# Kernel tuning notes

Hardware: AMD Instinct MI355X
Metric: run time of the kernel (lower is better)

Reference implementation:

```python
import jax, jax.numpy as jnp
import numpy as np

NUM_GROUPS = 32
EPS = 1e-6


def setup_inputs() -> dict:
    key = jax.random.key(0)
    ks = jax.random.split(key, 11)
    b, c, h, w = 4, 512, 64, 64
    s = 0.02
    return {
        "x": jax.random.normal(ks[0], (b, c, h, w), dtype=jnp.float32),
        "gn_w": jnp.ones((c,), dtype=jnp.float32),
        "gn_b": jnp.zeros((c,), dtype=jnp.float32),
        "wq": jax.random.normal(ks[1], (c, c), dtype=jnp.float32) * s,
        "bq": jax.random.normal(ks[2], (c,), dtype=jnp.float32) * s,
        "wk": jax.random.normal(ks[3], (c, c), dtype=jnp.float32) * s,
        "bk": jax.random.normal(ks[4], (c,), dtype=jnp.float32) * s,
        "wv": jax.random.normal(ks[5], (c, c), dtype=jnp.float32) * s,
        "bv": jax.random.normal(ks[6], (c,), dtype=jnp.float32) * s,
        "wo": jax.random.normal(ks[7], (c, c), dtype=jnp.float32) * s,
        "bo": jax.random.normal(ks[8], (c,), dtype=jnp.float32) * s,
    }


def _group_norm(x, gamma, beta):
    b, c, h, w = x.shape
    g = NUM_GROUPS
    xg = x.reshape(b, g, c // g, h, w)
    mean = jnp.mean(xg, axis=(2, 3, 4), keepdims=True)
    var = jnp.var(xg, axis=(2, 3, 4), keepdims=True)
    xg = (xg - mean) * jax.lax.rsqrt(var + EPS)
    x = xg.reshape(b, c, h, w)
    return x * gamma[None, :, None, None] + beta[None, :, None, None]


def _conv1x1(x, wmat, bias):
    # x: [b,c,h,w], wmat: [out,in] -> [b,out,h,w]
    return jnp.einsum('bchw,oc->bohw', x, wmat) + bias[None, :, None, None]


def reference(x, gn_w, gn_b, wq, bq, wk, bk, wv, bv, wo, bo):
    b, c, h, w = x.shape
    h_ = _group_norm(x, gn_w, gn_b)
    q = _conv1x1(h_, wq, bq).reshape(b, c, h * w)  # [b,c,hw]
    k = _conv1x1(h_, wk, bk).reshape(b, c, h * w)
    v = _conv1x1(h_, wv, bv).reshape(b, c, h * w)
    scale = float(c) ** (-0.5)
    # scores[b,i,j] = sum_c q[b,c,i] * k[b,c,j]
    scores = jnp.einsum('bci,bcj->bij', q, k) * scale
    attn = jax.nn.softmax(scores, axis=2)  # softmax over j (keys)
    # out[b,c,i] = sum_j v[b,c,j] * attn[b,i,j]
    out = jnp.einsum('bcj,bij->bci', v, attn).reshape(b, c, h, w)
    out = _conv1x1(out, wo, bo)
    return x + out
```

## Files before the change

kernel.cpp:

```cpp
#include <hip/hip_runtime.h>
#include <math.h>

using short8 = __attribute__((ext_vector_type(8))) short;
using f32x4  = __attribute__((ext_vector_type(4))) float;
using llong2 = __attribute__((ext_vector_type(2))) long long;
using i32x8  = __attribute__((ext_vector_type(8))) int;

__device__ __forceinline__ ushort f2bf(float f) {
    union { float f; uint u; } c; c.f = f;
    uint u = c.u;
    uint r = (u + 0x7FFFu + ((u >> 16) & 1u)) >> 16;
    return (ushort)r;
}
__device__ __forceinline__ float bf2f(ushort h) {
    union { uint u; float f; } c; c.u = ((uint)h) << 16;
    return c.f;
}
__device__ __forceinline__ uint pk4_fp8(float a, float b, float c, float d) {
    int v = __builtin_amdgcn_cvt_pk_fp8_f32(a, b, 0, false);
    v = __builtin_amdgcn_cvt_pk_fp8_f32(c, d, v, true);
    return (uint)v;
}
__device__ __forceinline__ unsigned char f2fp8(float x) {
    return (unsigned char)__builtin_amdgcn_cvt_pk_fp8_f32(x, 0.f, 0, false);
}

__device__ __forceinline__ void gload16(const void* g, void* l) {
    __builtin_amdgcn_global_load_lds(
        (const __attribute__((address_space(1))) unsigned int*)g,
        (__attribute__((address_space(3))) unsigned int*)l,
        16, 0, 0);
}

__global__ __launch_bounds__(256) void prep_weights(
    const float* __restrict__ wq, const float* __restrict__ bq,
    const float* __restrict__ wk, const float* __restrict__ bk,
    const float* __restrict__ wv, const float* __restrict__ wo,
    ushort* __restrict__ Wqk, ushort* __restrict__ Wv, ushort* __restrict__ Wo,
    float* __restrict__ bqk, float* __restrict__ stats, float scale)
{
    int idx = blockIdx.x * 256 + threadIdx.x;
    if (idx < 1024 * 512) {
        float v = (idx < 262144) ? wq[idx] * scale : wk[idx - 262144];
        Wqk[idx] = f2bf(v);
    }
    if (idx < 262144) {
        Wv[idx] = f2bf(wv[idx]);
        Wo[idx] = f2bf(wo[idx]);
    }
    if (idx < 1024) bqk[idx] = (idx < 512) ? bq[idx] * scale : bk[idx - 512];
    if (idx < 256) stats[idx] = 0.f;
}

__global__ __launch_bounds__(256) void gn_stats(
    const float* __restrict__ x, float* __restrict__ stats)
{
    int blk = blockIdx.x;
    int grp = blk >> 3, sub = blk & 7;
    const float* xp = x + (size_t)grp * 65536 + sub * 8192;
    int tid = threadIdx.x;

    float s = 0.f, sq = 0.f;
    #pragma unroll
    for (int j = 0; j < 8; ++j) {
        float4 v = *(const float4*)&xp[tid * 4 + j * 1024];
        s  += v.x + v.y + v.z + v.w;
        sq += v.x * v.x + v.y * v.y + v.z * v.z + v.w * v.w;
    }
    #pragma unroll
    for (int off = 32; off; off >>= 1) {
        s  += __shfl_xor(s,  off, 64);
        sq += __shfl_xor(sq, off, 64);
    }
    __shared__ float red[8];
    if ((tid & 63) == 0) { red[(tid >> 6) * 2] = s; red[(tid >> 6) * 2 + 1] = sq; }
    __syncthreads();
    if (tid == 0) {
        atomicAdd(&stats[grp * 2],     red[0] + red[2] + red[4] + red[6]);
        atomicAdd(&stats[grp * 2 + 1], red[1] + red[3] + red[5] + red[7]);
    }
}

__global__ __launch_bounds__(256) void gn_apply(
    const float* __restrict__ x, const float* __restrict__ gamma,
    const float* __restrict__ beta, const float* __restrict__ stats,
    ushort* __restrict__ hnt)
{
    int blk = blockIdx.x;
    int grp = blk >> 4, tile = blk & 15;
    int b = grp >> 5, g = grp & 31;
    const float* xp = x + (size_t)grp * 65536;
    int tid = threadIdx.x;

    float mean = stats[grp * 2] * (1.f / 65536.f);
    float var  = stats[grp * 2 + 1] * (1.f / 65536.f) - mean * mean;
    float rstd = rsqrtf(var + 1e-6f);

    int i0 = tile * 256;
    __shared__ ushort ls[16][256];
    #pragma unroll
    for (int ch = 0; ch < 16; ++ch) {
        float a = rstd * gamma[g * 16 + ch];
        float c = beta[g * 16 + ch] - mean * a;
        ls[ch][tid] = f2bf(xp[ch * 4096 + i0 + tid] * a + c);
    }
    __syncthreads();
    ushort t[16];
    #pragma unroll
    for (int ch = 0; ch < 16; ++ch) t[ch] = ls[ch][tid];
    size_t dst = ((size_t)b * 4096 + i0 + tid) * 512 + g * 16;
    *(uint4*)&hnt[dst]     = *(const uint4*)&t[0];
    *(uint4*)&hnt[dst + 8] = *(const uint4*)&t[8];
}

__global__ __launch_bounds__(256) void softmax_kernel(
    const ushort* __restrict__ S, unsigned char* __restrict__ P8)
{
    size_t row = blockIdx.x;
    const ushort* p = S + row * 4096;
    int tid = threadIdx.x;

    ushort tmp[16];
    *(uint4*)&tmp[0] = *(const uint4*)&p[tid * 16];
    *(uint4*)&tmp[8] = *(const uint4*)&p[tid * 16 + 8];
    float v[16];
    float mx = -1e30f;
    #pragma unroll
    for (int j = 0; j < 16; ++j) { v[j] = bf2f(tmp[j]); mx = fmaxf(mx, v[j]); }
    #pragma unroll
    for (int off = 32; off; off >>= 1) mx = fmaxf(mx, __shfl_xor(mx, off, 64));
    __shared__ float ls[8];
    if ((tid & 63) == 0) ls[tid >> 6] = mx;
    __syncthreads();
    float m4 = fmaxf(fmaxf(ls[0], ls[1]), fmaxf(ls[2], ls[3]));
    float sum = 0.f;
    #pragma unroll
    for (int j = 0; j < 16; ++j) { v[j] = __expf(v[j] - m4); sum += v[j]; }
    #pragma unroll
    for (int off = 32; off; off >>= 1) sum += __shfl_xor(sum, off, 64);
    if ((tid & 63) == 0) ls[4 + (tid >> 6)] = sum;
    __syncthreads();
    float inv = 256.0f / (ls[4] + ls[5] + ls[6] + ls[7]);
    int u = tid & 3;
    size_t base = row * 4096 + (size_t)(tid >> 2) * 64
                + (u & 1) * 32 + (u >> 1) * 8;
    uint2 o0, o1;
    o0.x = pk4_fp8(v[0] * inv,  v[1] * inv,  v[2] * inv,  v[3] * inv);
    o0.y = pk4_fp8(v[4] * inv,  v[5] * inv,  v[6] * inv,  v[7] * inv);
    o1.x = pk4_fp8(v[8] * inv,  v[9] * inv,  v[10] * inv, v[11] * inv);
    o1.y = pk4_fp8(v[12] * inv, v[13] * inv, v[14] * inv, v[15] * inv);
    *(uint2*)&P8[base]      = o0;
    *(uint2*)&P8[base + 16] = o1;
}

template <int BIAS, int OUT>
__global__ __launch_bounds__(256, 4) void gemm_nt(
    const ushort* __restrict__ Ag, const ushort* __restrict__ Bg,
    void* __restrict__ Cv, void* __restrict__ Cv2,
    const float* __restrict__ bias, const float* __restrict__ resid,
    int N, int K, int lda, int ldb,
    long sA, long sB, long sC)
{
    const int bz = blockIdx.z;
    Ag += (size_t)bz * sA;
    Bg += (size_t)bz * sB;

    const int tid  = threadIdx.x;
    const int wave = tid >> 6, lane = tid & 63;
    const int q = lane >> 4, lr = lane & 15;
    const int m0 = blockIdx.x * 128, n0 = blockIdx.y * 128;
    const int wm = (wave >> 1) * 64, wn = (wave & 1) * 64;

    __shared__ __align__(16) ushort As[2][128 * 32];
    __shared__ __align__(16) ushort Bs[2][128 * 32];

    const int srow = wave * 32 + (lane >> 2);
    const int skc  = (lane & 3) << 3;
    const size_t aoff0 = (size_t)(m0 + srow) * lda + skc;
    const size_t aoff1 = aoff0 + (size_t)16 * lda;
    const size_t boff0 = (size_t)(n0 + srow) * ldb + skc;
    const size_t boff1 = boff0 + (size_t)16 * ldb;
    const int l0 = wave * 1024, l1 = wave * 1024 + 512;

    f32x4 acc[4][4] = {};

    for (int kb = 0; kb < K; kb += 64) {
        __syncthreads();
        gload16(&Ag[aoff0 + kb],      &As[0][l0]);
        gload16(&Ag[aoff1 + kb],      &As[0][l1]);
        gload16(&Ag[aoff0 + kb + 32], &As[1][l0]);
        gload16(&Ag[aoff1 + kb + 32], &As[1][l1]);
        gload16(&Bg[boff0 + kb],      &Bs[0][l0]);
        gload16(&Bg[boff1 + kb],      &Bs[0][l1]);
        gload16(&Bg[boff0 + kb + 32], &Bs[1][l0]);
        gload16(&Bg[boff1 + kb + 32], &Bs[1][l1]);
        __syncthreads();

        #pragma unroll
        for (int kh = 0; kh < 2; ++kh) {
            short8 af[4], bfr[4];
            #pragma unroll
            for (int mt = 0; mt < 4; ++mt)
                af[mt] = *(const short8*)&As[kh][(wm + mt * 16 + lr) * 32 + q * 8];
            #pragma unroll
            for (int nt = 0; nt < 4; ++nt)
                bfr[nt] = *(const short8*)&Bs[kh][(wn + nt * 16 + lr) * 32 + q * 8];
            #pragma unroll
            for (int mt = 0; mt < 4; ++mt)
                #pragma unroll
                for (int nt = 0; nt < 4; ++nt)
                    acc[mt][nt] = __builtin_amdgcn_mfma_f32_16x16x32_bf16(
                        af[mt], bfr[nt], acc[mt][nt], 0, 0, 0);
        }
    }

    #pragma unroll
    for (int mt = 0; mt < 4; ++mt) {
        int rb = m0 + wm + mt * 16 + q * 4;
        #pragma unroll
        for (int nt = 0; nt < 4; ++nt) {
            int cn = n0 + wn + nt * 16 + lr;
            #pragma unroll
            for (int t = 0; t < 4; ++t) {
                int r = rb + t;
                float v = acc[mt][nt][t];
                if (BIAS == 1) v += bias[r];
                if (BIAS == 2) v += bias[cn];
                if (OUT == 1) {
                    size_t o = (size_t)bz * sC + (size_t)r * N + cn;
                    ((float*)Cv)[o] = v + resid[o];
                } else if (OUT == 2) {
                    int w = cn & 63, a = w >> 3;
                    int sp = (cn & ~63) | ((a & 3) * 16 + (a >> 2) * 8 + (w & 7));
                    ((unsigned char*)Cv)[(size_t)bz * sC + (size_t)r * N + sp] =
                        f2fp8(v);
                } else if (OUT == 3) {
                    if (cn < 512)
                        ((unsigned char*)Cv)[(size_t)bz * sC + (size_t)r * 512 + cn]
                            = f2fp8(v * 16.f);
                    else
                        ((unsigned char*)Cv2)[(size_t)bz * sC + (size_t)r * 512 + (cn - 512)]
                            = f2fp8(v);
                } else {
                    size_t o = (size_t)bz * sC + (size_t)r * N + cn;
                    ((ushort*)Cv)[o] = f2bf(v);
                }
            }
        }
    }
}

__global__ __launch_bounds__(256, 2) void gemm_qk(
    const unsigned char* __restrict__ Q8, const unsigned char* __restrict__ K8,
    ushort* __restrict__ S)
{
    const int bz = blockIdx.z;
    const unsigned char* Ag = Q8 + (size_t)bz * 2097152;
    const unsigned char* Bg = K8 + (size_t)bz * 2097152;

    const int tid  = threadIdx.x;
    const int wave = tid >> 6, lane = tid & 63;
    const int q = lane >> 4, lr = lane & 15;
    const int m0 = blockIdx.x * 128, n0 = blockIdx.y * 128;
    const int wm = (wave >> 1) * 64, wn = (wave & 1) * 64;

    __shared__ __align__(16) unsigned char As[128 * 128];
    __shared__ __align__(16) unsigned char Bs[128 * 128];

    const int lrow = lane >> 3;
    const size_t laneoff = (size_t)lrow * 512 + ((lane & 7) ^ (lrow & 7)) * 16;
    const size_t abase = (size_t)(m0 + wave * 32) * 512 + laneoff;
    const size_t bbase = (size_t)(n0 + wave * 32) * 512 + laneoff;
    unsigned char* lA = &As[wave * 32 * 128];
    unsigned char* lB = &Bs[wave * 32 * 128];

    const int e0 = (2 * q) ^ (lr & 7), e1 = e0 ^ 1;

    f32x4 acc[4][4] = {};
    const int sA = 0x7B7B7B7B;
    const int sB = 0x7F7F7F7F;

    for (int kb = 0; kb < 512; kb += 128) {
        __syncthreads();
        #pragma unroll
        for (int t = 0; t < 4; ++t) {
            gload16(Ag + abase + (size_t)t * 4096 + kb, lA + t * 1024);
            gload16(Bg + bbase + (size_t)t * 4096 + kb, lB + t * 1024);
        }
        __syncthreads();

        i32x8 af[4], bf[4];
        #pragma unroll
        for (int mt = 0; mt < 4; ++mt) {
            int r = wm + mt * 16 + lr;
            union { uint4 v[2]; i32x8 f; } u;
            u.v[0] = *(const uint4*)&As[r * 128 + e0 * 16];
            u.v[1] = *(const uint4*)&As[r * 128 + e1 * 16];
            af[mt] = u.f;
        }
        #pragma unroll
        for (int nt = 0; nt < 4; ++nt) {
            int r = wn + nt * 16 + lr;
            union { uint4 v[2]; i32x8 f; } u;
            u.v[0] = *(const uint4*)&Bs[r * 128 + e0 * 16];
            u.v[1] = *(const uint4*)&Bs[r * 128 + e1 * 16];
            bf[nt] = u.f;
        }
        #pragma unroll
        for (int mt = 0; mt < 4; ++mt)
            #pragma unroll
            for (int nt = 0; nt < 4; ++nt)
                acc[mt][nt] = __builtin_amdgcn_mfma_scale_f32_16x16x128_f8f6f4(
                    af[mt], bf[nt], acc[mt][nt], 0, 0, 0, sA, 0, sB);
    }

    #pragma unroll
    for (int mt = 0; mt < 4; ++mt) {
        int rb = m0 + wm + mt * 16 + q * 4;
        #pragma unroll
        for (int nt = 0; nt < 4; ++nt) {
            int cn = n0 + wn + nt * 16 + lr;
            #pragma unroll
            for (int t = 0; t < 4; ++t) {
                size_t o = (size_t)bz * 16777216 + (size_t)(rb + t) * 4096 + cn;
                S[o] = f2bf(acc[mt][nt][t]);
            }
        }
    }
}

__global__ __launch_bounds__(256, 4) void gemm_pv(
    const unsigned char* __restrict__ P8, const unsigned char* __restrict__ V8,
    ushort* __restrict__ Ot)
{
    const int bz = blockIdx.z;
    const unsigned char* Ag = P8 + (size_t)bz * 16777216;
    const unsigned char* Bg = V8 + (size_t)bz * 2097152;

    const int tid  = threadIdx.x;
    const int wave = tid >> 6, lane = tid & 63;
    const int q = lane >> 4, lr = lane & 15;
    const int m0 = blockIdx.x * 128, n0 = blockIdx.y * 128;
    const int wm = (wave >> 1) * 64, wn = (wave & 1) * 64;

    __shared__ __align__(16) unsigned char As[2][128 * 64];
    __shared__ __align__(16) unsigned char Bs[2][128 * 64];

    const int srow = wave * 32 + (lane >> 2);
    const int soff = (lane & 3) << 4;
    const size_t a0 = (size_t)(m0 + srow) * 4096 + soff;
    const size_t a1 = a0 + (size_t)16 * 4096;
    const size_t b0 = (size_t)(n0 + srow) * 4096 + soff;
    const size_t b1 = b0 + (size_t)16 * 4096;
    const int l0 = wave * 2048, l1 = wave * 2048 + 1024;

    f32x4 acc[4][4] = {};

    for (int kb = 0; kb < 4096; kb += 128) {
        __syncthreads();
        gload16(Ag + a0 + kb,      &As[0][l0]);
        gload16(Ag + a1 + kb,      &As[0][l1]);
        gload16(Ag + a0 + kb + 64, &As[1][l0]);
        gload16(Ag + a1 + kb + 64, &As[1][l1]);
        gload16(Bg + b0 + kb,      &Bs[0][l0]);
        gload16(Bg + b1 + kb,      &Bs[0][l1]);
        gload16(Bg + b0 + kb + 64, &Bs[1][l0]);
        gload16(Bg + b1 + kb + 64, &Bs[1][l1]);
        __syncthreads();

        #pragma unroll
        for (int kh = 0; kh < 2; ++kh) {
            llong2 af[4], bf[4];
            #pragma unroll
            for (int mt = 0; mt < 4; ++mt)
                af[mt] = *(const llong2*)
                    &As[kh][(wm + mt * 16 + lr) * 64 + q * 16];
            #pragma unroll
            for (int nt = 0; nt < 4; ++nt)
                bf[nt] = *(const llong2*)
                    &Bs[kh][(wn + nt * 16 + lr) * 64 + q * 16];
            #pragma unroll
            for (int mt = 0; mt < 4; ++mt)
                #pragma unroll
                for (int nt = 0; nt < 4; ++nt)
                    acc[mt][nt] = __builtin_amdgcn_mfma_f32_16x16x32_fp8_fp8(
                        af[mt].x, bf[nt].x, acc[mt][nt], 0, 0, 0);
            #pragma unroll
            for (int mt = 0; mt < 4; ++mt)
                #pragma unroll
                for (int nt = 0; nt < 4; ++nt)
                    acc[mt][nt] = __builtin_amdgcn_mfma_f32_16x16x32_fp8_fp8(
                        af[mt].y, bf[nt].y, acc[mt][nt], 0, 0, 0);
        }
    }

    #pragma unroll
    for (int mt = 0; mt < 4; ++mt) {
        int rb = m0 + wm + mt * 16 + q * 4;
        #pragma unroll
        for (int nt = 0; nt < 4; ++nt) {
            int cn = n0 + wn + nt * 16 + lr;
            #pragma unroll
            for (int t = 0; t < 4; ++t) {
                size_t o = (size_t)bz * 2097152 + (size_t)(rb + t) * 512 + cn;
                Ot[o] = f2bf(acc[mt][nt][t] * (1.f / 256.f));
            }
        }
    }
}

extern "C" void kernel_launch(void* const* d_in, const int* in_sizes, int n_in,
                              void* d_out, int out_size, void* d_ws, size_t ws_size,
                              hipStream_t stream)
{
    const float* x   = (const float*)d_in[0];
    const float* gnw = (const float*)d_in[1];
    const float* gnb = (const float*)d_in[2];
    const float* wq  = (const float*)d_in[3];
    const float* bq  = (const float*)d_in[4];
    const float* wk  = (const float*)d_in[5];
    const float* bk  = (const float*)d_in[6];
    const float* wv  = (const float*)d_in[7];
    const float* bv  = (const float*)d_in[8];
    const float* wo  = (const float*)d_in[9];
    const float* bo  = (const float*)d_in[10];
    float* out = (float*)d_out;

    char* ws = (char*)d_ws;
    ushort*        S   = (ushort*)(ws);
    ushort*        Ot  = (ushort*)(ws);
    ushort*        hnt = (ushort*)(ws + 134217728);
    unsigned char* Q8  = (unsigned char*)(ws + 150994944);
    unsigned char* K8  = (unsigned char*)(ws + 159383552);
    unsigned char* P8  = (unsigned char*)(ws + 134217728);
    unsigned char* V8  = (unsigned char*)(ws + 201326592);
    ushort*        Wqk = (ushort*)(ws + 209715200);
    ushort*        Wv  = (ushort*)(ws + 210763776);
    ushort*        Wo  = (ushort*)(ws + 211288064);
    float*         bqk = (float*) (ws + 211812352);
    float*         st  = (float*) (ws + 211816448);

    const float scale = 1.0f / sqrtf(512.0f);
    const long sHW  = 512L * 4096;

    prep_weights<<<2048, 256, 0, stream>>>(wq, bq, wk, bk, wv, wo,
                                           Wqk, Wv, Wo, bqk, st, scale);
    gn_stats<<<1024, 256, 0, stream>>>(x, st);
    gn_apply<<<2048, 256, 0, stream>>>(x, gnw, gnb, st, hnt);

    gemm_nt<2, 3><<<dim3(32, 8, 4), 256, 0, stream>>>(
        hnt, Wqk, Q8, K8, bqk, nullptr,
        1024, 512, 512, 512, sHW, 0L, sHW);

    gemm_nt<1, 2><<<dim3(4, 32, 4), 256, 0, stream>>>(
        Wv, hnt, V8, nullptr, bv, nullptr,
        4096, 512, 512, 512, 0L, sHW, sHW);

    gemm_qk<<<dim3(32, 32, 4), 256, 0, stream>>>(Q8, K8, S);

    softmax_kernel<<<16384, 256, 0, stream>>>(S, P8);

    gemm_pv<<<dim3(32, 4, 4), 256, 0, stream>>>(P8, V8, Ot);

    gemm_nt<1, 1><<<dim3(4, 32, 4), 256, 0, stream>>>(
        Wo, Ot, out, nullptr, bo, x,
        4096, 512, 512, 512, 0L, sHW, sHW);
}
```

Before: 305.7 us.

## Double-buffer QK and PV GEMMs and switch PV to scaled 128-K fp8 MFMA

The QK GEMM gains double-buffered LDS staging, so the next K tile is loaded while the current one is being multiplied. The PV GEMM is rewritten to match: XOR-swizzled 128-wide tiles, double buffering, and the scaled 16x16x128 f8f6f4 MFMA. Its scale exponent now folds in the 1/256 factor, so the epilogue multiply is removed. The softmax and V producers drop their interleaved byte permutation and write plain row-major layout. PV occupancy bounds fall from 4 to 2 because each block now uses 64KB of LDS.

```diff
diff --git a/kernel.cpp b/kernel.cpp
--- a/kernel.cpp
+++ b/kernel.cpp
@@ -141,16 +141,14 @@
     if ((tid & 63) == 0) ls[4 + (tid >> 6)] = sum;
     __syncthreads();
     float inv = 256.0f / (ls[4] + ls[5] + ls[6] + ls[7]);
-    int u = tid & 3;
-    size_t base = row * 4096 + (size_t)(tid >> 2) * 64
-                + (u & 1) * 32 + (u >> 1) * 8;
+    size_t base = row * 4096 + (size_t)tid * 16;
     uint2 o0, o1;
     o0.x = pk4_fp8(v[0] * inv,  v[1] * inv,  v[2] * inv,  v[3] * inv);
     o0.y = pk4_fp8(v[4] * inv,  v[5] * inv,  v[6] * inv,  v[7] * inv);
     o1.x = pk4_fp8(v[8] * inv,  v[9] * inv,  v[10] * inv, v[11] * inv);
     o1.y = pk4_fp8(v[12] * inv, v[13] * inv, v[14] * inv, v[15] * inv);
-    *(uint2*)&P8[base]      = o0;
-    *(uint2*)&P8[base + 16] = o1;
+    *(uint2*)&P8[base]     = o0;
+    *(uint2*)&P8[base + 8] = o1;
 }
 
 template <int BIAS, int OUT>
@@ -230,9 +228,7 @@
                     size_t o = (size_t)bz * sC + (size_t)r * N + cn;
                     ((float*)Cv)[o] = v + resid[o];
                 } else if (OUT == 2) {
-                    int w = cn & 63, a = w >> 3;
-                    int sp = (cn & ~63) | ((a & 3) * 16 + (a >> 2) * 8 + (w & 7));
-                    ((unsigned char*)Cv)[(size_t)bz * sC + (size_t)r * N + sp] =
+                    ((unsigned char*)Cv)[(size_t)bz * sC + (size_t)r * N + cn] =
                         f2fp8(v);
                 } else if (OUT == 3) {
                     if (cn < 512)
@@ -264,15 +260,14 @@
     const int m0 = blockIdx.x * 128, n0 = blockIdx.y * 128;
     const int wm = (wave >> 1) * 64, wn = (wave & 1) * 64;
 
-    __shared__ __align__(16) unsigned char As[128 * 128];
-    __shared__ __align__(16) unsigned char Bs[128 * 128];
+    __shared__ __align__(16) unsigned char As[2][128 * 128];
+    __shared__ __align__(16) unsigned char Bs[2][128 * 128];
 
     const int lrow = lane >> 3;
     const size_t laneoff = (size_t)lrow * 512 + ((lane & 7) ^ (lrow & 7)) * 16;
     const size_t abase = (size_t)(m0 + wave * 32) * 512 + laneoff;
     const size_t bbase = (size_t)(n0 + wave * 32) * 512 + laneoff;
-    unsigned char* lA = &As[wave * 32 * 128];
-    unsigned char* lB = &Bs[wave * 32 * 128];
+    const int lbase = wave * 32 * 128;
 
     const int e0 = (2 * q) ^ (lr & 7), e1 = e0 ^ 1;
 
@@ -280,30 +275,36 @@
     const int sA = 0x7B7B7B7B;
     const int sB = 0x7F7F7F7F;
 
-    for (int kb = 0; kb < 512; kb += 128) {
-        __syncthreads();
+    auto stage = [&](int kb, int buf) {
         #pragma unroll
         for (int t = 0; t < 4; ++t) {
-            gload16(Ag + abase + (size_t)t * 4096 + kb, lA + t * 1024);
-            gload16(Bg + bbase + (size_t)t * 4096 + kb, lB + t * 1024);
-        }
-        __syncthreads();
+            gload16(Ag + abase + (size_t)t * 4096 + kb, &As[buf][lbase + t * 1024]);
+            gload16(Bg + bbase + (size_t)t * 4096 + kb, &Bs[buf][lbase + t * 1024]);
+        }
+    };
+
+    stage(0, 0);
+    __syncthreads();
+
+    for (int it = 0; it < 4; ++it) {
+        const int cur = it & 1;
+        if (it < 3) stage((it + 1) * 128, cur ^ 1);
 
         i32x8 af[4], bf[4];
         #pragma unroll
         for (int mt = 0; mt < 4; ++mt) {
             int r = wm + mt * 16 + lr;
             union { uint4 v[2]; i32x8 f; } u;
-            u.v[0] = *(const uint4*)&As[r * 128 + e0 * 16];
-            u.v[1] = *(const uint4*)&As[r * 128 + e1 * 16];
+            u.v[0] = *(const uint4*)&As[cur][r * 128 + e0 * 16];
+            u.v[1] = *(const uint4*)&As[cur][r * 128 + e1 * 16];
             af[mt] = u.f;
         }
         #pragma unroll
         for (int nt = 0; nt < 4; ++nt) {
             int r = wn + nt * 16 + lr;
             union { uint4 v[2]; i32x8 f; } u;
-            u.v[0] = *(const uint4*)&Bs[r * 128 + e0 * 16];
-            u.v[1] = *(const uint4*)&Bs[r * 128 + e1 * 16];
+            u.v[0] = *(const uint4*)&Bs[cur][r * 128 + e0 * 16];
+            u.v[1] = *(const uint4*)&Bs[cur][r * 128 + e1 * 16];
             bf[nt] = u.f;
         }
         #pragma unroll
@@ -312,6 +313,8 @@
             for (int nt = 0; nt < 4; ++nt)
                 acc[mt][nt] = __builtin_amdgcn_mfma_scale_f32_16x16x128_f8f6f4(
                     af[mt], bf[nt], acc[mt][nt], 0, 0, 0, sA, 0, sB);
+
+        __syncthreads();
     }
 
     #pragma unroll
@@ -329,7 +332,7 @@
     }
 }
 
-__global__ __launch_bounds__(256, 4) void gemm_pv(
+__global__ __launch_bounds__(256, 2) void gemm_pv(
     const unsigned char* __restrict__ P8, const unsigned char* __restrict__ V8,
     ushort* __restrict__ Ot)
 {
@@ -343,55 +346,61 @@
     const int m0 = blockIdx.x * 128, n0 = blockIdx.y * 128;
     const int wm = (wave >> 1) * 64, wn = (wave & 1) * 64;
 
-    __shared__ __align__(16) unsigned char As[2][128 * 64];
-    __shared__ __align__(16) unsigned char Bs[2][128 * 64];
-
-    const int srow = wave * 32 + (lane >> 2);
-    const int soff = (lane & 3) << 4;
-    const size_t a0 = (size_t)(m0 + srow) * 4096 + soff;
-    const size_t a1 = a0 + (size_t)16 * 4096;
-    const size_t b0 = (size_t)(n0 + srow) * 4096 + soff;
-    const size_t b1 = b0 + (size_t)16 * 4096;
-    const int l0 = wave * 2048, l1 = wave * 2048 + 1024;
+    __shared__ __align__(16) unsigned char As[2][128 * 128];
+    __shared__ __align__(16) unsigned char Bs[2][128 * 128];
+
+    const int lrow = lane >> 3;
+    const size_t laneoff = (size_t)lrow * 4096 + ((lane & 7) ^ (lrow & 7)) * 16;
+    const size_t abase = (size_t)(m0 + wave * 32) * 4096 + laneoff;
+    const size_t bbase = (size_t)(n0 + wave * 32) * 4096 + laneoff;
+    const int lbase = wave * 32 * 128;
+
+    const int e0 = (2 * q) ^ (lr & 7), e1 = e0 ^ 1;
 
     f32x4 acc[4][4] = {};
-
-    for (int kb = 0; kb < 4096; kb += 128) {
+    const int sA = 0x77777777;
+    const int sB = 0x7F7F7F7F;
+
+    auto stage = [&](int kb, int buf) {
+        #pragma unroll
+        for (int t = 0; t < 4; ++t) {
+            gload16(Ag + abase + (size_t)t * 32768 + kb, &As[buf][lbase + t * 1024]);
+            gload16(Bg + bbase + (size_t)t * 32768 + kb, &Bs[buf][lbase + t * 1024]);
+        }
+    };
+
+    stage(0, 0);
+    __syncthreads();
+
+    for (int it = 0; it < 32; ++it) {
+        const int cur = it & 1;
+        if (it < 31) stage((it + 1) * 128, cur ^ 1);
+
+        i32x8 af[4], bf[4];
+        #pragma unroll
+        for (int mt = 0; mt < 4; ++mt) {
+            int r = wm + mt * 16 + lr;
+            union { uint4 v[2]; i32x8 f; } u;
+            u.v[0] = *(const uint4*)&As[cur][r * 128 + e0 * 16];
+            u.v[1] = *(const uint4*)&As[cur][r * 128 + e1 * 16];
+            af[mt] = u.f;
+        }
+        #pragma unroll
+        for (int nt = 0; nt < 4; ++nt) {
+            int r = wn + nt * 16 + lr;
+            union { uint4 v[2]; i32x8 f; } u;
+            u.v[0] = *(const uint4*)&Bs[cur][r * 128 + e0 * 16];
+            u.v[1] = *(const uint4*)&Bs[cur][r * 128 + e1 * 16];
+            bf[nt] = u.f;
+        }
+        #pragma unroll
+        for (int mt = 0; mt < 4; ++mt)
+            #pragma unroll
+            for (int nt = 0; nt < 4; ++nt)
+                acc[mt][nt] = __builtin_amdgcn_mfma_scale_f32_16x16x128_f8f6f4(
+                    af[mt], bf[nt], acc[mt][nt], 0, 0, 0, sA, 0, sB);
+
         __syncthreads();
-        gload16(Ag + a0 + kb,      &As[0][l0]);
-        gload16(Ag + a1 + kb,      &As[0][l1]);
-        gload16(Ag + a0 + kb + 64, &As[1][l0]);
-        gload16(Ag + a1 + kb + 64, &As[1][l1]);
-        gload16(Bg + b0 + kb,      &Bs[0][l0]);
-        gload16(Bg + b1 + kb,      &Bs[0][l1]);
-        gload16(Bg + b0 + kb + 64, &Bs[1][l0]);
-        gload16(Bg + b1 + kb + 64, &Bs[1][l1]);
-        __syncthreads();
-
-        #pragma unroll
-        for (int kh = 0; kh < 2; ++kh) {
-            llong2 af[4], bf[4];
-            #pragma unroll
-            for (int mt = 0; mt < 4; ++mt)
-                af[mt] = *(const llong2*)
-                    &As[kh][(wm + mt * 16 + lr) * 64 + q * 16];
-            #pragma unroll
-            for (int nt = 0; nt < 4; ++nt)
-                bf[nt] = *(const llong2*)
-                    &Bs[kh][(wn + nt * 16 + lr) * 64 + q * 16];
-            #pragma unroll
-            for (int mt = 0; mt < 4; ++mt)
-                #pragma unroll
-                for (int nt = 0; nt < 4; ++nt)
-                    acc[mt][nt] = __builtin_amdgcn_mfma_f32_16x16x32_fp8_fp8(
-                        af[mt].x, bf[nt].x, acc[mt][nt], 0, 0, 0);
-            #pragma unroll
-            for (int mt = 0; mt < 4; ++mt)
-                #pragma unroll
-                for (int nt = 0; nt < 4; ++nt)
-                    acc[mt][nt] = __builtin_amdgcn_mfma_f32_16x16x32_fp8_fp8(
-                        af[mt].y, bf[nt].y, acc[mt][nt], 0, 0, 0);
-        }
     }
 
     #pragma unroll
@@ -403,7 +412,7 @@
             #pragma unroll
             for (int t = 0; t < 4; ++t) {
                 size_t o = (size_t)bz * 2097152 + (size_t)(rb + t) * 512 + cn;
-                Ot[o] = f2bf(acc[mt][nt][t] * (1.f / 256.f));
+                Ot[o] = f2bf(acc[mt][nt][t]);
             }
         }
     }
```

After: 301.9 us. Within noise of the previous version (-1.2%).
